# Kernel tuning notes

Hardware: AMD Instinct MI355X
Metric: run time of the kernel (lower is better)

Reference implementation:

```python
import jax, jax.numpy as jnp
import numpy as np
from jax import lax


def haar_dwt2(x):
    """Level-1 Haar (db1) 2D DWT on [N, H, W] with even H, W.
    Returns cA, cH, cV (cD is discarded by the module), each [N, H//2, W//2].
    Matches pywt/ptwt db1 block form: cA=(a+b+c+d)/2, etc."""
    a = x[:, 0::2, 0::2]
    b = x[:, 0::2, 1::2]
    c = x[:, 1::2, 0::2]
    d = x[:, 1::2, 1::2]
    cA = (a + b + c + d) * 0.5
    cH = (a + b - c - d) * 0.5  # horizontal detail (highpass along rows axis)
    cV = (a - b + c - d) * 0.5  # vertical detail (highpass along cols axis)
    return cA, cH, cV


def conv2d_same(x, w, b):
    # x: [N, Cin, H, W], w: [Cout, Cin, kh, kw]
    y = lax.conv_general_dilated(x, w, window_strides=(1, 1), padding='SAME',
                                 dimension_numbers=('NCHW', 'OIHW', 'NCHW'))
    return y + b[None, :, None, None]


def maxpool2(x):
    return lax.reduce_window(x, -jnp.inf, lax.max,
                             window_dimensions=(1, 1, 2, 2),
                             window_strides=(1, 1, 2, 2), padding='VALID')


def setup_inputs() -> dict:
    key = jax.random.key(0)
    ks = jax.random.split(key, 7)
    B, C, H, W = 32, 3, 512, 512
    x = jax.random.normal(ks[0], (B, C, H, W), dtype=jnp.float32)
    # conv stack params (Conv2d(1,16,3), Conv2d(16,8,3), Conv2d(8,4,1))
    w1 = jax.random.normal(ks[1], (16, 1, 3, 3), dtype=jnp.float32) * (1.0 / 3.0)
    b1 = jnp.zeros((16,), dtype=jnp.float32)
    w2 = jax.random.normal(ks[2], (8, 16, 3, 3), dtype=jnp.float32) * (1.0 / 12.0)
    b2 = jnp.zeros((8,), dtype=jnp.float32)
    w3 = jax.random.normal(ks[3], (4, 8, 1, 1), dtype=jnp.float32) * (1.0 / 2.83)
    b3 = jnp.zeros((4,), dtype=jnp.float32)
    return {"x": x, "w1": w1, "b1": b1, "w2": w2, "b2": b2, "w3": w3, "b3": b3}


def reference(x, w1, b1, w2, b2, w3, b3):
    B, C, H, W = x.shape
    # Batch the per-image/per-channel loop: treat each channel as one map.
    flat = x.reshape(B * C, H, W)
    cA, cH, cV = haar_dwt2(flat)  # [B*C, H/2, W/2]

    # Low-frequency conv stack on approx coeffs (1 input channel per map).
    h = cA[:, None, :, :]                       # [B*C, 1, H/2, W/2]
    h = maxpool2(jax.nn.relu(conv2d_same(h, w1, b1)))
    h = maxpool2(jax.nn.relu(conv2d_same(h, w2, b2)))
    h = conv2d_same(h, w3, b3)                  # [B*C, 4, H/8, W/8]
    # per-channel flatten, then concat over channels (dim=1 in the original)
    low = h.reshape(B, 1, -1)                   # [B, 1, C*4*(H/8)*(W/8)]

    # High-frequency: per channel concat [cH.flatten(), cV.flatten()],
    # then concat over channels.
    n = (H // 2) * (W // 2)
    high = jnp.concatenate([cH.reshape(B, C, n), cV.reshape(B, C, n)], axis=-1)
    high = high.reshape(B, 1, C * 2 * n)        # [B, 1, C*2*(H/2)*(W/2)]
    return low, high
```

## Files before the change

kernel.cpp:

```cpp
#include <hip/hip_runtime.h>


__global__ __launch_bounds__(256, 4) void fused_all_kernel(
    const float* __restrict__ x,
    const float* __restrict__ w1, const float* __restrict__ b1,
    const float* __restrict__ w2, const float* __restrict__ b2,
    const float* __restrict__ w3, const float* __restrict__ b3,
    float* __restrict__ outLow, float* __restrict__ outHigh)
{
    __shared__ __align__(16) float ca[70 * 72];
    __shared__ __align__(16) float h1s[4 * 34 * 36];

    int img = blockIdx.x >> 4;
    int t   = blockIdx.x & 15;
    int ty = t >> 2, tx = t & 3;
    int hy0 = ty * 32 - 1, hx0 = tx * 32 - 1;
    int cy0 = ty * 64 - 3, cx0 = tx * 64 - 3;

    const float* xi = x + img * 262144;
    float* hb = outHigh + img * 131072;

    #pragma unroll
    for (int k = 0; k < 4; ++k) {
        int i = threadIdx.x + k * 256;
        int row = i >> 4, cg = i & 15;
        int gy = ty * 64 + row;
        int gx = tx * 64 + cg * 4;
        const float* r0 = xi + (2 * gy) * 512 + 2 * gx;
        const float* r1 = r0 + 512;
        float4 t0 = *(const float4*)(r0);
        float4 t1 = *(const float4*)(r0 + 4);
        float4 u0 = *(const float4*)(r1);
        float4 u1 = *(const float4*)(r1 + 4);
        float4 vA, vH, vV;
        vA.x = (t0.x + t0.y + u0.x + u0.y) * 0.5f;
        vH.x = (t0.x + t0.y - u0.x - u0.y) * 0.5f;
        vV.x = (t0.x - t0.y + u0.x - u0.y) * 0.5f;
        vA.y = (t0.z + t0.w + u0.z + u0.w) * 0.5f;
        vH.y = (t0.z + t0.w - u0.z - u0.w) * 0.5f;
        vV.y = (t0.z - t0.w + u0.z - u0.w) * 0.5f;
        vA.z = (t1.x + t1.y + u1.x + u1.y) * 0.5f;
        vH.z = (t1.x + t1.y - u1.x - u1.y) * 0.5f;
        vV.z = (t1.x - t1.y + u1.x - u1.y) * 0.5f;
        vA.w = (t1.z + t1.w + u1.z + u1.w) * 0.5f;
        vH.w = (t1.z + t1.w - u1.z - u1.w) * 0.5f;
        vV.w = (t1.z - t1.w + u1.z - u1.w) * 0.5f;
        int po = (gy << 8) + gx;
        *(float4*)(hb + po) = vH;
        *(float4*)(hb + 65536 + po) = vV;
        float* cp = ca + (row + 3) * 72 + cg * 4 + 3;
        cp[0] = vA.x; cp[1] = vA.y; cp[2] = vA.z; cp[3] = vA.w;
    }

    for (int i = threadIdx.x; i < 804; i += 256) {
        int r, c;
        if (i < 210)      { r = i / 70;              c = i - r * 70; }
        else if (i < 420) { int j = i - 210; r = 67 + j / 70; c = j - (j / 70) * 70; }
        else              { int j = i - 420; r = 3 + j / 6; int k6 = j - (j / 6) * 6;
                            c = (k6 < 3) ? k6 : (64 + k6); }
        int gy = cy0 + r, gx = cx0 + c;
        float v = 0.f;
        if ((unsigned)gy < 256u && (unsigned)gx < 256u) {
            const float* p0 = xi + (2 * gy) * 512 + 2 * gx;
            float2 a = *(const float2*)(p0);
            float2 b = *(const float2*)(p0 + 512);
            v = (a.x + a.y + b.x + b.y) * 0.5f;
        }
        ca[r * 72 + c] = v;
    }

    int ly = threadIdx.x >> 4, lx = threadIdx.x & 15;
    float acc[8][2][2];
    #pragma unroll
    for (int oc = 0; oc < 8; ++oc)
        #pragma unroll
        for (int r = 0; r < 2; ++r)
            #pragma unroll
            for (int c = 0; c < 2; ++c) acc[oc][r][c] = 0.f;

    __syncthreads();

    #pragma unroll 1
    for (int cc = 0; cc < 4; ++cc) {
        float wk1[4][9], bb1[4];
        #pragma unroll
        for (int o = 0; o < 4; ++o) {
            #pragma unroll
            for (int k = 0; k < 9; ++k) wk1[o][k] = w1[(cc * 4 + o) * 9 + k];
            bb1[o] = b1[cc * 4 + o];
        }
        if (cc) __syncthreads();

        #pragma unroll 1
        for (int k = 0; k < 5; ++k) {
            int i = threadIdx.x + k * 256;
            if (i < 1156) {
                int hy = i / 34, hx = i - hy * 34;
                const float* pb = ca + (2 * hy) * 72 + 2 * hx;
                float patch[4][4];
                #pragma unroll
                for (int r = 0; r < 4; ++r) {
                    float2 a = *(const float2*)(pb + r * 72);
                    float2 b = *(const float2*)(pb + r * 72 + 2);
                    patch[r][0] = a.x; patch[r][1] = a.y;
                    patch[r][2] = b.x; patch[r][3] = b.y;
                }
                bool oob = ((unsigned)(hy0 + hy) >= 128u) | ((unsigned)(hx0 + hx) >= 128u);
                #pragma unroll
                for (int o = 0; o < 4; ++o) {
                    float p00 = 0.f, p01 = 0.f, p10 = 0.f, p11 = 0.f;
                    #pragma unroll
                    for (int ky = 0; ky < 3; ++ky)
                        #pragma unroll
                        for (int kx = 0; kx < 3; ++kx) {
                            float wv = wk1[o][ky * 3 + kx];
                            p00 += patch[ky][kx]         * wv;
                            p01 += patch[ky][kx + 1]     * wv;
                            p10 += patch[ky + 1][kx]     * wv;
                            p11 += patch[ky + 1][kx + 1] * wv;
                        }
                    float m = fmaxf(fmaxf(p00, p01), fmaxf(p10, p11)) + bb1[o];
                    m = fmaxf(m, 0.f);
                    h1s[(o * 34 + hy) * 36 + hx] = oob ? 0.f : m;
                }
            }
        }
        __syncthreads();

        #pragma unroll
        for (int icl = 0; icl < 4; ++icl) {
            float win[4][4];
            const float* base = h1s + (icl * 34 + ly * 2) * 36 + lx * 2;
            #pragma unroll
            for (int r = 0; r < 4; ++r) {
                float2 p = *(const float2*)(base + r * 36);
                float2 q = *(const float2*)(base + r * 36 + 2);
                win[r][0] = p.x; win[r][1] = p.y; win[r][2] = q.x; win[r][3] = q.y;
            }
            int ic = cc * 4 + icl;
            #pragma unroll
            for (int oc = 0; oc < 8; ++oc) {
                const float* wb = w2 + (oc * 16 + ic) * 9;
                #pragma unroll
                for (int ky = 0; ky < 3; ++ky)
                    #pragma unroll
                    for (int kx = 0; kx < 3; ++kx) {
                        float wv = wb[ky * 3 + kx];
                        #pragma unroll
                        for (int r = 0; r < 2; ++r)
                            #pragma unroll
                            for (int c = 0; c < 2; ++c)
                                acc[oc][r][c] += win[r + ky][c + kx] * wv;
                    }
            }
        }
    }

    float h2v[8];
    #pragma unroll
    for (int oc = 0; oc < 8; ++oc) {
        float m = fmaxf(fmaxf(acc[oc][0][0], acc[oc][0][1]),
                        fmaxf(acc[oc][1][0], acc[oc][1][1]));
        h2v[oc] = fmaxf(m + b2[oc], 0.f);
    }
    float* dst = outLow + img * 16384;
    int pos = (ty * 16 + ly) * 64 + tx * 16 + lx;
    #pragma unroll
    for (int oc3 = 0; oc3 < 4; ++oc3) {
        float s = b3[oc3];
        #pragma unroll
        for (int ic = 0; ic < 8; ++ic) s += w3[oc3 * 8 + ic] * h2v[ic];
        dst[oc3 * 4096 + pos] = s;
    }
}

extern "C" void kernel_launch(void* const* d_in, const int* in_sizes, int n_in,
                              void* d_out, int out_size, void* d_ws, size_t ws_size,
                              hipStream_t stream) {
    const float* x  = (const float*)d_in[0];
    const float* w1 = (const float*)d_in[1];
    const float* b1 = (const float*)d_in[2];
    const float* w2 = (const float*)d_in[3];
    const float* b2 = (const float*)d_in[4];
    const float* w3 = (const float*)d_in[5];
    const float* b3 = (const float*)d_in[6];
    float* out     = (float*)d_out;
    float* outLow  = out;
    float* outHigh = out + 1572864;

    fused_all_kernel<<<1536, 256, 0, stream>>>(x, w1, b1, w2, b2, w3, b3,
                                               outLow, outHigh);
}
```

Before: 238.9 us.

## Compute second conv with fp16 MFMA using channel-interleaved fp16 h1 tile

The second 3x3 conv (16→8 channels) now runs as an implicit GEMM on MFMA 16x16x32 f16 instructions instead of scalar FMAs. The h1 intermediate is stored in shared memory as fp16 with channels interleaved (8 per pixel), and the conv1 stage runs in two chunks of 8 channels instead of four chunks of 4. The pooled conv2 results go through shared memory before the 1x1 conv. This cuts the FMA-bound conv2 work but lowers h1 precision to fp16, pads half of each MFMA's N dimension with zero weights, and lowers launch bounds from 4 to 3 blocks per SIMD.

Result: slower. 251.0 us (+5.1%).

```diff
diff --git a/kernel.cpp b/kernel.cpp
--- a/kernel.cpp
+++ b/kernel.cpp
@@ -1,15 +1,18 @@
 #include <hip/hip_runtime.h>
 
 
-__global__ __launch_bounds__(256, 4) void fused_all_kernel(
+typedef _Float16 f16x8 __attribute__((ext_vector_type(8)));
+typedef float    f32x4 __attribute__((ext_vector_type(4)));
+
+__global__ __launch_bounds__(256, 3) void fused_all_kernel(
     const float* __restrict__ x,
     const float* __restrict__ w1, const float* __restrict__ b1,
     const float* __restrict__ w2, const float* __restrict__ b2,
     const float* __restrict__ w3, const float* __restrict__ b3,
     float* __restrict__ outLow, float* __restrict__ outHigh)
 {
-    __shared__ __align__(16) float ca[70 * 72];
-    __shared__ __align__(16) float h1s[4 * 34 * 36];
+    __shared__ __align__(16) float    ca[70 * 72];
+    __shared__ __align__(16) _Float16 h1s[38 * 36 * 8];
 
     int img = blockIdx.x >> 4;
     int t   = blockIdx.x & 15;
@@ -19,6 +22,30 @@
 
     const float* xi = x + img * 262144;
     float* hb = outHigh + img * 131072;
+
+    int lane = threadIdx.x & 63;
+    int wid  = threadIdx.x >> 6;
+    int q = lane >> 4, m = lane & 15;
+    int ppy = m >> 2, ppx = m & 3;
+    int wy = wid >> 1, wx = wid & 1;
+
+    f16x8 Bf[2][3];
+    #pragma unroll
+    for (int c = 0; c < 2; ++c)
+        #pragma unroll
+        for (int s = 0; s < 3; ++s) {
+            f16x8 bf;
+            #pragma unroll
+            for (int j = 0; j < 8; ++j) {
+                int tt = s * 4 + q;
+                float wvv = 0.f;
+                if (m < 8 && tt < 9) wvv = w2[(m * 16 + (c * 8 + j)) * 9 + tt];
+                bf[j] = (_Float16)wvv;
+            }
+            Bf[c][s] = bf;
+        }
+    float bb2 = 0.f;
+    if (m < 8) bb2 = b2[m];
 
     #pragma unroll
     for (int k = 0; k < 4; ++k) {
@@ -69,26 +96,31 @@
         ca[r * 72 + c] = v;
     }
 
-    int ly = threadIdx.x >> 4, lx = threadIdx.x & 15;
-    float acc[8][2][2];
-    #pragma unroll
-    for (int oc = 0; oc < 8; ++oc)
-        #pragma unroll
-        for (int r = 0; r < 2; ++r)
-            #pragma unroll
-            for (int c = 0; c < 2; ++c) acc[oc][r][c] = 0.f;
+    {
+        f16x8 z;
+        #pragma unroll
+        for (int j = 0; j < 8; ++j) z[j] = (_Float16)0.f;
+        for (int i = threadIdx.x; i < 144; i += 256)
+            *(f16x8*)(h1s + (34 * 36 + i) * 8) = z;
+    }
+
+    int ky0 = (q >= 3) ? 1 : 0, kx0 = (q >= 3) ? 0 : q;
+    int t1q = q + 4;
+    int ky1 = (t1q >= 6) ? 2 : 1, kx1 = t1q - ky1 * 3;
+    int off0 = ((ppy + ky0) * 36 + (ppx + kx0)) * 8;
+    int off1 = ((ppy + ky1) * 36 + (ppx + kx1)) * 8;
+    int off2 = ((ppy + 2) * 36 + (ppx + 2)) * 8;
+    int zoff = ((34 + ppy) * 36 + ppx) * 8;
+    bool z2 = (q != 0);
+
+    f32x4 acc[16];
+    #pragma unroll
+    for (int i = 0; i < 16; ++i) acc[i] = (f32x4){0.f, 0.f, 0.f, 0.f};
 
     __syncthreads();
 
-    #pragma unroll 1
-    for (int cc = 0; cc < 4; ++cc) {
-        float wk1[4][9], bb1[4];
-        #pragma unroll
-        for (int o = 0; o < 4; ++o) {
-            #pragma unroll
-            for (int k = 0; k < 9; ++k) wk1[o][k] = w1[(cc * 4 + o) * 9 + k];
-            bb1[o] = b1[cc * 4 + o];
-        }
+    #pragma unroll
+    for (int cc = 0; cc < 2; ++cc) {
         if (cc) __syncthreads();
 
         #pragma unroll 1
@@ -106,71 +138,81 @@
                     patch[r][2] = b.x; patch[r][3] = b.y;
                 }
                 bool oob = ((unsigned)(hy0 + hy) >= 128u) | ((unsigned)(hx0 + hx) >= 128u);
+                f16x8 ov;
                 #pragma unroll
-                for (int o = 0; o < 4; ++o) {
-                    float p00 = 0.f, p01 = 0.f, p10 = 0.f, p11 = 0.f;
+                for (int og = 0; og < 2; ++og) {
                     #pragma unroll
-                    for (int ky = 0; ky < 3; ++ky)
+                    for (int o = 0; o < 4; ++o) {
+                        int oc = cc * 8 + og * 4 + o;
+                        float p00 = 0.f, p01 = 0.f, p10 = 0.f, p11 = 0.f;
                         #pragma unroll
-                        for (int kx = 0; kx < 3; ++kx) {
-                            float wv = wk1[o][ky * 3 + kx];
-                            p00 += patch[ky][kx]         * wv;
-                            p01 += patch[ky][kx + 1]     * wv;
-                            p10 += patch[ky + 1][kx]     * wv;
-                            p11 += patch[ky + 1][kx + 1] * wv;
-                        }
-                    float m = fmaxf(fmaxf(p00, p01), fmaxf(p10, p11)) + bb1[o];
-                    m = fmaxf(m, 0.f);
-                    h1s[(o * 34 + hy) * 36 + hx] = oob ? 0.f : m;
+                        for (int ky = 0; ky < 3; ++ky)
+                            #pragma unroll
+                            for (int kx = 0; kx < 3; ++kx) {
+                                float wvv = w1[oc * 9 + ky * 3 + kx];
+                                p00 += patch[ky][kx]         * wvv;
+                                p01 += patch[ky][kx + 1]     * wvv;
+                                p10 += patch[ky + 1][kx]     * wvv;
+                                p11 += patch[ky + 1][kx + 1] * wvv;
+                            }
+                        float mm = fmaxf(fmaxf(p00, p01), fmaxf(p10, p11)) + b1[oc];
+                        mm = fmaxf(mm, 0.f);
+                        ov[og * 4 + o] = (_Float16)(oob ? 0.f : mm);
+                    }
                 }
+                *(f16x8*)(h1s + (hy * 36 + hx) * 8) = ov;
             }
         }
         __syncthreads();
 
         #pragma unroll
-        for (int icl = 0; icl < 4; ++icl) {
-            float win[4][4];
-            const float* base = h1s + (icl * 34 + ly * 2) * 36 + lx * 2;
+        for (int mt = 0; mt < 16; ++mt) {
+            int my = mt >> 2, mx = mt & 3;
+            int pbase = ((wy * 16 + my * 4) * 36 + (wx * 16 + mx * 4)) * 8;
+            f16x8 a0 = *(const f16x8*)(h1s + pbase + off0);
+            f16x8 a1 = *(const f16x8*)(h1s + pbase + off1);
+            int a2i = z2 ? zoff : (pbase + off2);
+            f16x8 a2 = *(const f16x8*)(h1s + a2i);
+            acc[mt] = __builtin_amdgcn_mfma_f32_16x16x32_f16(a0, Bf[cc][0], acc[mt], 0, 0, 0);
+            acc[mt] = __builtin_amdgcn_mfma_f32_16x16x32_f16(a1, Bf[cc][1], acc[mt], 0, 0, 0);
+            acc[mt] = __builtin_amdgcn_mfma_f32_16x16x32_f16(a2, Bf[cc][2], acc[mt], 0, 0, 0);
+        }
+    }
+
+    float* h2b = (float*)ca;
+    #pragma unroll
+    for (int mt = 0; mt < 16; ++mt) {
+        int my = mt >> 2, mx = mt & 3;
+        float u0 = fmaxf(acc[mt][0], acc[mt][1]);
+        float u1 = fmaxf(acc[mt][2], acc[mt][3]);
+        float v0 = fmaxf(u0, __shfl_xor(u0, 16, 64));
+        float v1 = fmaxf(u1, __shfl_xor(u1, 16, 64));
+        float h20 = fmaxf(v0 + bb2, 0.f);
+        float h21 = fmaxf(v1 + bb2, 0.f);
+        if (m < 8 && (q & 1) == 0) {
+            int Yp = wy * 8 + my * 2 + (q >> 1);
+            int Xp = wx * 8 + mx * 2;
+            h2b[(Yp * 16 + Xp) * 8 + m]     = h20;
+            h2b[(Yp * 16 + Xp + 1) * 8 + m] = h21;
+        }
+    }
+    __syncthreads();
+
+    {
+        int Yp = threadIdx.x >> 4, Xp = threadIdx.x & 15;
+        const float* hv = h2b + (Yp * 16 + Xp) * 8;
+        float4 va = *(const float4*)(hv);
+        float4 vb = *(const float4*)(hv + 4);
+        float h2v[8] = {va.x, va.y, va.z, va.w, vb.x, vb.y, vb.z, vb.w};
+        float* dst = outLow + img * 16384;
+        int pos = (ty * 16 + Yp) * 64 + tx * 16 + Xp;
+        #pragma unroll
+        for (int oc3 = 0; oc3 < 4; ++oc3) {
+            float s = b3[oc3];
             #pragma unroll
-            for (int r = 0; r < 4; ++r) {
-                float2 p = *(const float2*)(base + r * 36);
-                float2 q = *(const float2*)(base + r * 36 + 2);
-                win[r][0] = p.x; win[r][1] = p.y; win[r][2] = q.x; win[r][3] = q.y;
-            }
-            int ic = cc * 4 + icl;
-            #pragma unroll
-            for (int oc = 0; oc < 8; ++oc) {
-                const float* wb = w2 + (oc * 16 + ic) * 9;
-                #pragma unroll
-                for (int ky = 0; ky < 3; ++ky)
-                    #pragma unroll
-                    for (int kx = 0; kx < 3; ++kx) {
-                        float wv = wb[ky * 3 + kx];
-                        #pragma unroll
-                        for (int r = 0; r < 2; ++r)
-                            #pragma unroll
-                            for (int c = 0; c < 2; ++c)
-                                acc[oc][r][c] += win[r + ky][c + kx] * wv;
-                    }
-            }
-        }
-    }
-
-    float h2v[8];
-    #pragma unroll
-    for (int oc = 0; oc < 8; ++oc) {
-        float m = fmaxf(fmaxf(acc[oc][0][0], acc[oc][0][1]),
-                        fmaxf(acc[oc][1][0], acc[oc][1][1]));
-        h2v[oc] = fmaxf(m + b2[oc], 0.f);
-    }
-    float* dst = outLow + img * 16384;
-    int pos = (ty * 16 + ly) * 64 + tx * 16 + lx;
-    #pragma unroll
-    for (int oc3 = 0; oc3 < 4; ++oc3) {
-        float s = b3[oc3];
-        #pragma unroll
-        for (int ic = 0; ic < 8; ++ic) s += w3[oc3 * 8 + ic] * h2v[ic];
-        dst[oc3 * 4096 + pos] = s;
+            for (int ic = 0; ic < 8; ++ic) s += w3[oc3 * 8 + ic] * h2v[ic];
+            dst[oc3 * 4096 + pos] = s;
+        }
     }
 }
 
```
